# Performance work log

Hardware: AMD Instinct MI355X
Metric: run time of the kernel (lower is better)

## Reference

```python
import jax, jax.numpy as jnp
import numpy as np

B, C, N, K = 16, 128, 16384, 64  # point clouds, feat dim, points per cloud, clusters per cloud


def setup_inputs() -> dict:
    key = jax.random.key(0)
    k1, k2, k3 = jax.random.split(key, 3)
    point_features = jax.random.normal(k1, (B, C, N), dtype=jnp.float32)
    cluster_ids = jax.random.randint(k2, (B, N), 0, K, dtype=jnp.int32)
    # labels of the clusters common across augmented views; drawn from the same label space
    common_cluster_ids = jax.random.randint(k3, (B, K), 0, K, dtype=jnp.int32)
    return {
        "point_features": point_features,
        "cluster_ids": cluster_ids,
        "common_cluster_ids": common_cluster_ids,
    }


def reference(point_features, cluster_ids, common_cluster_ids):
    """Cluster branch of ProjectionPointHead.forward.

    Original: for each point cloud, for each common cluster label, boolean-mask
    the (C, n_seg) point features and max_pool1d over the segment, then vstack.
    Here: one fused segmented max per point cloud, then gather the common labels.
    Output matches torch.vstack(batch_seg_feats): (B*K, C).
    """
    def per_pc(pf, cids, common):
        # pf: (C, N) -> (N, C); segmented max over points -> (K, C)
        seg_max = jax.ops.segment_max(pf.T, cids, num_segments=K)
        return seg_max[common]  # (K_common, C)

    feats = jax.vmap(per_pc)(point_features, cluster_ids, common_cluster_ids)  # (B, K, C)
    return feats.reshape(-1, feats.shape[-1])
```

## Files before the change

kernel.cpp:

```cpp
#include <hip/hip_runtime.h>

#define B 16
#define C 128
#define N 16384
#define K 64

#define CT 32
#define NB 2048
#define LDS_STRIDE 33

#define ENC_NEG_INF 0x007FFFFFu

__device__ __forceinline__ unsigned enc(float f) {
    unsigned u = __float_as_uint(f);
    return (u & 0x80000000u) ? ~u : (u | 0x80000000u);
}
__device__ __forceinline__ float dec(unsigned u) {
    unsigned v = (u & 0x80000000u) ? (u & 0x7FFFFFFFu) : ~u;
    return __uint_as_float(v);
}

__global__ void seg_init(unsigned* __restrict__ gseg) {
    int i = blockIdx.x * blockDim.x + threadIdx.x;
    if (i < B * K * C) gseg[i] = ENC_NEG_INF;
}

__global__ __launch_bounds__(256) void seg_scatter(const float* __restrict__ pf,
                                                   const int* __restrict__ ids,
                                                   unsigned* __restrict__ gseg) {
    __shared__ unsigned lds[K * LDS_STRIDE];
    const int tid = threadIdx.x;
    const int b  = blockIdx.z;
    const int c0 = blockIdx.y * CT;
    const int n0 = blockIdx.x * NB;

    for (int i = tid; i < K * LDS_STRIDE; i += 256) lds[i] = ENC_NEG_INF;

    const int4* ids4 = reinterpret_cast<const int4*>(ids + b * N + n0);
    const int4 ka = ids4[tid];
    const int4 kb = ids4[tid + 256];
    __syncthreads();

    const float* base = pf + ((size_t)b * C + c0) * N + n0;
#pragma unroll 4
    for (int c = 0; c < CT; ++c) {
        const float4* src = reinterpret_cast<const float4*>(base + (size_t)c * N);
        float4 va = src[tid];
        float4 vb = src[tid + 256];
        atomicMax(&lds[ka.x * LDS_STRIDE + c], enc(va.x));
        atomicMax(&lds[ka.y * LDS_STRIDE + c], enc(va.y));
        atomicMax(&lds[ka.z * LDS_STRIDE + c], enc(va.z));
        atomicMax(&lds[ka.w * LDS_STRIDE + c], enc(va.w));
        atomicMax(&lds[kb.x * LDS_STRIDE + c], enc(vb.x));
        atomicMax(&lds[kb.y * LDS_STRIDE + c], enc(vb.y));
        atomicMax(&lds[kb.z * LDS_STRIDE + c], enc(vb.z));
        atomicMax(&lds[kb.w * LDS_STRIDE + c], enc(vb.w));
    }
    __syncthreads();

    for (int i = tid; i < K * CT; i += 256) {
        int k = i / CT, c = i % CT;
        unsigned v = lds[k * LDS_STRIDE + c];
        if (v != ENC_NEG_INF)
            atomicMax(&gseg[((size_t)(b * K + k)) * C + c0 + c], v);
    }
}

__global__ void seg_gather(const unsigned* __restrict__ gseg,
                           const int* __restrict__ common,
                           float* __restrict__ out) {
    int i = blockIdx.x * blockDim.x + threadIdx.x;
    if (i >= B * K * C) return;
    int c = i % C;
    int row = i / C;
    int b = row / K;
    int cid = common[row];
    out[i] = dec(gseg[((size_t)(b * K + cid)) * C + c]);
}

extern "C" void kernel_launch(void* const* d_in, const int* in_sizes, int n_in,
                              void* d_out, int out_size, void* d_ws, size_t ws_size,
                              hipStream_t stream) {
    const float* pf     = (const float*)d_in[0];
    const int*   ids    = (const int*)d_in[1];
    const int*   common = (const int*)d_in[2];
    float* out = (float*)d_out;
    unsigned* gseg = (unsigned*)d_ws;

    const int total = B * K * C;
    seg_init<<<(total + 255) / 256, 256, 0, stream>>>(gseg);

    dim3 grid(N / NB, C / CT, B);
    seg_scatter<<<grid, 256, 0, stream>>>(pf, ids, gseg);

    seg_gather<<<(total + 255) / 256, 256, 0, stream>>>(gseg, common, out);
}
```

Before: 208.0 us.

## Replace global atomics with per-chunk partials and fused reduce-gather kernel

Drops the init kernel and the global atomicMax merge. Each block now writes its LDS segment-max tile to a private partial buffer, and a second kernel reduces the 16 chunk partials only for the gathered common cluster rows, using vectorized loads. The scatter block size is halved to 1024 points per block, doubling the grid, and the next channel row is software-prefetched. This removes one launch and global atomic contention, but adds partial-buffer traffic and halves the work per block.

Result: faster. 195.4 us (-6.1%).

```diff
diff --git a/kernel.cpp b/kernel.cpp
--- a/kernel.cpp
+++ b/kernel.cpp
@@ -6,8 +6,10 @@
 #define K 64
 
 #define CT 32
-#define NB 2048
-#define LDS_STRIDE 33
+#define NCH 16
+#define NB (N / NCH)
+#define NCT (C / CT)
+#define LDSS 33
 
 #define ENC_NEG_INF 0x007FFFFFu
 
@@ -20,62 +22,66 @@
     return __uint_as_float(v);
 }
 
-__global__ void seg_init(unsigned* __restrict__ gseg) {
-    int i = blockIdx.x * blockDim.x + threadIdx.x;
-    if (i < B * K * C) gseg[i] = ENC_NEG_INF;
-}
-
 __global__ __launch_bounds__(256) void seg_scatter(const float* __restrict__ pf,
                                                    const int* __restrict__ ids,
-                                                   unsigned* __restrict__ gseg) {
-    __shared__ unsigned lds[K * LDS_STRIDE];
-    const int tid = threadIdx.x;
-    const int b  = blockIdx.z;
-    const int c0 = blockIdx.y * CT;
-    const int n0 = blockIdx.x * NB;
+                                                   unsigned* __restrict__ part) {
+    __shared__ unsigned lds[K * LDSS];
+    const int tid   = threadIdx.x;
+    const int chunk = blockIdx.x;
+    const int ct    = blockIdx.y;
+    const int b     = blockIdx.z;
+    const int c0    = ct * CT;
+    const int n0    = chunk * NB;
 
-    for (int i = tid; i < K * LDS_STRIDE; i += 256) lds[i] = ENC_NEG_INF;
+    for (int i = tid; i < K * LDSS; i += 256) lds[i] = ENC_NEG_INF;
 
-    const int4* ids4 = reinterpret_cast<const int4*>(ids + b * N + n0);
-    const int4 ka = ids4[tid];
-    const int4 kb = ids4[tid + 256];
+    const int4 kk = reinterpret_cast<const int4*>(ids + b * N + n0)[tid];
+    const int kx = kk.x * LDSS, ky = kk.y * LDSS, kz = kk.z * LDSS, kw = kk.w * LDSS;
     __syncthreads();
 
     const float* base = pf + ((size_t)b * C + c0) * N + n0;
-#pragma unroll 4
+    float4 cur = reinterpret_cast<const float4*>(base)[tid];
+#pragma unroll
     for (int c = 0; c < CT; ++c) {
-        const float4* src = reinterpret_cast<const float4*>(base + (size_t)c * N);
-        float4 va = src[tid];
-        float4 vb = src[tid + 256];
-        atomicMax(&lds[ka.x * LDS_STRIDE + c], enc(va.x));
-        atomicMax(&lds[ka.y * LDS_STRIDE + c], enc(va.y));
-        atomicMax(&lds[ka.z * LDS_STRIDE + c], enc(va.z));
-        atomicMax(&lds[ka.w * LDS_STRIDE + c], enc(va.w));
-        atomicMax(&lds[kb.x * LDS_STRIDE + c], enc(vb.x));
-        atomicMax(&lds[kb.y * LDS_STRIDE + c], enc(vb.y));
-        atomicMax(&lds[kb.z * LDS_STRIDE + c], enc(vb.z));
-        atomicMax(&lds[kb.w * LDS_STRIDE + c], enc(vb.w));
+        float4 nxt = cur;
+        if (c + 1 < CT)
+            nxt = reinterpret_cast<const float4*>(base + (size_t)(c + 1) * N)[tid];
+        atomicMax(&lds[kx + c], enc(cur.x));
+        atomicMax(&lds[ky + c], enc(cur.y));
+        atomicMax(&lds[kz + c], enc(cur.z));
+        atomicMax(&lds[kw + c], enc(cur.w));
+        cur = nxt;
     }
     __syncthreads();
 
+    unsigned* dst = part + (((size_t)(b * NCT + ct) * NCH + chunk) * K) * CT;
     for (int i = tid; i < K * CT; i += 256) {
-        int k = i / CT, c = i % CT;
-        unsigned v = lds[k * LDS_STRIDE + c];
-        if (v != ENC_NEG_INF)
-            atomicMax(&gseg[((size_t)(b * K + k)) * C + c0 + c], v);
+        int k = i >> 5, cl = i & 31;
+        dst[i] = lds[k * LDSS + cl];
     }
 }
 
-__global__ void seg_gather(const unsigned* __restrict__ gseg,
-                           const int* __restrict__ common,
-                           float* __restrict__ out) {
-    int i = blockIdx.x * blockDim.x + threadIdx.x;
-    if (i >= B * K * C) return;
-    int c = i % C;
-    int row = i / C;
-    int b = row / K;
-    int cid = common[row];
-    out[i] = dec(gseg[((size_t)(b * K + cid)) * C + c]);
+__global__ __launch_bounds__(256) void seg_reduce(const unsigned* __restrict__ part,
+                                                  const int* __restrict__ common,
+                                                  float* __restrict__ out) {
+    const int i = blockIdx.x * blockDim.x + threadIdx.x;
+    if (i >= B * K * C / 4) return;
+    const int c0  = (i & 31) * 4;
+    const int row = i >> 5;
+    const int cid = common[row];
+    const int b   = row >> 6;
+    const int ct  = c0 >> 5, cl = c0 & 31;
+
+    const unsigned* p = part + (((size_t)(b * NCT + ct) * NCH) * K + cid) * CT + cl;
+    uint4 m = make_uint4(ENC_NEG_INF, ENC_NEG_INF, ENC_NEG_INF, ENC_NEG_INF);
+#pragma unroll
+    for (int ch = 0; ch < NCH; ++ch) {
+        uint4 v = *reinterpret_cast<const uint4*>(p + (size_t)ch * K * CT);
+        m.x = max(m.x, v.x); m.y = max(m.y, v.y);
+        m.z = max(m.z, v.z); m.w = max(m.w, v.w);
+    }
+    float4 o = make_float4(dec(m.x), dec(m.y), dec(m.z), dec(m.w));
+    reinterpret_cast<float4*>(out)[i] = o;
 }
 
 extern "C" void kernel_launch(void* const* d_in, const int* in_sizes, int n_in,
@@ -85,13 +91,11 @@
     const int*   ids    = (const int*)d_in[1];
     const int*   common = (const int*)d_in[2];
     float* out = (float*)d_out;
-    unsigned* gseg = (unsigned*)d_ws;
+    unsigned* part = (unsigned*)d_ws;
 
-    const int total = B * K * C;
-    seg_init<<<(total + 255) / 256, 256, 0, stream>>>(gseg);
+    dim3 grid(NCH, NCT, B);
+    seg_scatter<<<grid, 256, 0, stream>>>(pf, ids, part);
 
-    dim3 grid(N / NB, C / CT, B);
-    seg_scatter<<<grid, 256, 0, stream>>>(pf, ids, gseg);
-
-    seg_gather<<<(total + 255) / 256, 256, 0, stream>>>(gseg, common, out);
+    const int rtotal = B * K * C / 4;
+    seg_reduce<<<(rtotal + 255) / 256, 256, 0, stream>>>(part, common, out);
 }
```
